# Kernel optimization log

Measured on AMD Instinct MI355X. Metric: run time of the kernel, lower is better.

The kernel has to match this reference:

```python
import jax, jax.numpy as jnp
import numpy as np
from jax import lax

SIGMA = 10.0


def _maxpool3(x):
    # x: (1, N, D, H, W), kernel 3, stride 1, VALID
    return lax.reduce_window(x, -jnp.inf, lax.max,
                             (1, 1, 3, 3, 3), (1, 1, 1, 1, 1), 'VALID')


def _avgpool3(x):
    s = lax.reduce_window(x, 0.0, lax.add,
                          (1, 1, 3, 3, 3), (1, 1, 1, 1, 1), 'VALID')
    return s / 27.0


def _smooth(x):
    # ReplicationPad3d(3) -> MaxPool3d(3,1) -> AvgPool3d(3,1) x2 ; keeps spatial size
    x = jnp.pad(x, ((0, 0), (0, 0), (3, 3), (3, 3), (3, 3)), mode='edge')
    return _avgpool3(_avgpool3(_maxpool3(x)))


def setup_inputs() -> dict:
    key = jax.random.key(0)
    k1, k2, k3 = jax.random.split(key, 3)
    N, K, L = 10000, 8, 13
    cost = jax.random.normal(k1, (N, 1, L, L, L), dtype=jnp.float32)
    knn = jax.random.randint(k2, (N, K), 0, N)
    dist_nn = jax.random.uniform(k3, (N, K), dtype=jnp.float32) * 20.0
    alpha = jnp.array([1.0, 0.1, 1.0, 1.0, 0.1, 1.0], dtype=jnp.float32)
    return {"cost": cost, "knn": knn, "dist_nn": dist_nn, "alpha": alpha}


def reference(cost, knn, dist_nn, alpha):
    N = cost.shape[0]
    L = cost.shape[2]
    cost = alpha[1] + alpha[0] * cost                       # (N,1,L,L,L)
    w = jnp.exp(-dist_nn / (2.0 * SIGMA ** 2))              # (N,K)
    norm = w.sum(axis=1)                                    # (N,)
    cost = cost.reshape(1, N, L, L, L)

    cost_approx = _smooth(cost)                             # (1,N,L,L,L)
    # gather K neighbors and do distance-weighted mean
    nbr = cost_approx[:, knn]                               # (1,N,K,L,L,L)
    cost_approx = jnp.einsum('ankxyz,nk->anxyz', nbr, w)
    cost_approx = cost_approx / norm[None, :, None, None, None]

    cost = alpha[4] + alpha[2] * cost + alpha[3] * cost_approx
    cost = _smooth(cost)
    nbr = cost[:, knn]                                      # (1,N,K,L,L,L)
    cost = jnp.einsum('ankxyz,nk->anxyz', nbr, w)
    cost = cost / norm[None, :, None, None, None]
    return alpha[5] * cost.reshape(1, N, -1)
```

## Files before the change

### kernel.cpp

```cpp
#include <hip/hip_runtime.h>
#include <math.h>

#define L3 2197
#define SP 2200
#define NV (SP / 8)
#define NTW 64
#define NTO 320

#define SSZ 3760

typedef unsigned int u32;

__device__ __forceinline__ u32 pack2bf(float a, float b) {
    u32 ua = __float_as_uint(a);
    u32 ub = __float_as_uint(b);
    ua = (ua + 0x7fffu + ((ua >> 16) & 1u)) >> 16;
    ub = (ub + 0x7fffu + ((ub >> 16) & 1u)) & 0xffff0000u;
    return ua | ub;
}

__device__ __forceinline__ void unpack8(uint4 v, float* f) {
    f[0] = __uint_as_float(v.x << 16);
    f[1] = __uint_as_float(v.x & 0xffff0000u);
    f[2] = __uint_as_float(v.y << 16);
    f[3] = __uint_as_float(v.y & 0xffff0000u);
    f[4] = __uint_as_float(v.z << 16);
    f[5] = __uint_as_float(v.z & 0xffff0000u);
    f[6] = __uint_as_float(v.w << 16);
    f[7] = __uint_as_float(v.w & 0xffff0000u);
}

__device__ __forceinline__ uint4 pack8(const float* f) {
    uint4 v;
    v.x = pack2bf(f[0], f[1]);
    v.y = pack2bf(f[2], f[3]);
    v.z = pack2bf(f[4], f[5]);
    v.w = pack2bf(f[6], f[7]);
    return v;
}

__device__ __forceinline__ void maxpool_row(const float* x, float* o) {
    float p[12];
#pragma unroll
    for (int i = 0; i < 12; ++i) p[i] = fmaxf(x[i], x[i + 1]);
    o[0] = x[0];
    o[1] = x[0];
    o[2] = p[0];
#pragma unroll
    for (int j = 3; j <= 13; ++j) o[j] = fmaxf(p[j - 3], x[j - 1]);
    o[14] = p[11];
    o[15] = x[12];
    o[16] = x[12];
}

__device__ __forceinline__ void tri_row(const float* y, float* o, float scale) {
#pragma unroll
    for (int c = 0; c < 13; ++c) {
        float s = fmaf(2.0f, y[c + 1], y[c]);
        s = fmaf(3.0f, y[c + 2], s);
        s = fmaf(2.0f, y[c + 3], s);
        o[c] = (s + y[c + 4]) * scale;
    }
}

__device__ void smooth_wave(float* S, const int lane) {
    __syncthreads();
#pragma unroll
    for (int cb = 2; cb >= 0; --cb) {
        const int p = cb * 64 + lane;
        const bool act = p < 169;
        float x[13], o[17];
        if (act) {
            const float* s = S + p * 13;
#pragma unroll
            for (int i = 0; i < 13; ++i) x[i] = s[i];
            maxpool_row(x, o);
        }
        __builtin_amdgcn_sched_barrier(0);
        if (act) {
            float* d = S + p * 17;
#pragma unroll
            for (int i = 0; i < 17; ++i) d[i] = o[i];
        }
        __builtin_amdgcn_sched_barrier(0);
    }
    __syncthreads();
#pragma unroll
    for (int cb = 3; cb >= 0; --cb) {
        const int p = cb * 64 + lane;
        const bool act = p < 221;
        const int a = p / 17, c = p % 17;
        float x[13], o[17];
        if (act) {
            const float* s = S + a * 221 + c;
#pragma unroll
            for (int i = 0; i < 13; ++i) x[i] = s[i * 17];
            maxpool_row(x, o);
        }
        __builtin_amdgcn_sched_barrier(0);
        if (act) {
            float* d = S + a * 289 + c;
#pragma unroll
            for (int i = 0; i < 17; ++i) d[i * 17] = o[i];
        }
        __builtin_amdgcn_sched_barrier(0);
    }
    __syncthreads();
#pragma unroll
    for (int cb = 0; cb < 5; ++cb) {
        const int p = cb * 64 + lane;
        if (p < 289) {
            float x[13], m[17], o[13];
            const float* s = S + p;
#pragma unroll
            for (int i = 0; i < 13; ++i) x[i] = s[i * 289];
            maxpool_row(x, m);
            tri_row(m, o, 1.0f);
            float* d = S + p;
#pragma unroll
            for (int i = 0; i < 13; ++i) d[i * 289] = o[i];
        }
    }
    __syncthreads();
#pragma unroll
    for (int cb = 0; cb < 4; ++cb) {
        const int p = cb * 64 + lane;
        const bool act = p < 221;
        const int a = p / 17, c = p % 17;
        float y[17], o[13];
        if (act) {
            const float* s = S + a * 289 + c;
#pragma unroll
            for (int i = 0; i < 17; ++i) y[i] = s[i * 17];
            tri_row(y, o, 1.0f);
        }
        __builtin_amdgcn_sched_barrier(0);
        if (act) {
            float* d = S + a * 221 + c;
#pragma unroll
            for (int i = 0; i < 13; ++i) d[i * 17] = o[i];
        }
        __builtin_amdgcn_sched_barrier(0);
    }
    __syncthreads();
#pragma unroll
    for (int cb = 0; cb < 3; ++cb) {
        const int p = cb * 64 + lane;
        const bool act = p < 169;
        float y[17], o[13];
        if (act) {
            const float* s = S + p * 17;
#pragma unroll
            for (int i = 0; i < 17; ++i) y[i] = s[i];
            tri_row(y, o, 1.0f / 729.0f);
        }
        __builtin_amdgcn_sched_barrier(0);
        if (act) {
            float* d = S + p * 13;
#pragma unroll
            for (int i = 0; i < 13; ++i) d[i] = o[i];
        }
        __builtin_amdgcn_sched_barrier(0);
    }
    __syncthreads();
}

__device__ __forceinline__ void load_nbr_meta(
        const int* __restrict__ knn, const float* __restrict__ dist,
        int n, int K, int* idx, float* wk, float* norm_out) {
    float dv[8];
#pragma unroll
    for (int k = 0; k < 8; ++k) {
        const int kc = (k < K) ? k : (K - 1);
        idx[k] = knn[n * K + kc];
        dv[k] = dist[n * K + kc];
    }
    float norm = 0.0f;
#pragma unroll
    for (int k = 0; k < 8; ++k) {
        float w = (k < K) ? expf(-dv[k] * (1.0f / 200.0f)) : 0.0f;
        wk[k] = w;
        norm += w;
    }
    *norm_out = norm;
}

__global__ __launch_bounds__(NTW) void k_smooth1(
        const float* __restrict__ cost, const float* __restrict__ alpha,
        uint4* __restrict__ tmp1, uint4* __restrict__ preA) {
    __shared__ alignas(16) float S[SSZ];
    const int n = blockIdx.x;
    const int lane = threadIdx.x;
    const float a0 = alpha[0], a1 = alpha[1], a2 = alpha[2], a4 = alpha[4];
    const float* src = cost + (size_t)n * L3;
    for (int i = lane; i < L3; i += NTW) S[i] = fmaf(a0, src[i], a1);
    if (lane < SP - L3) S[L3 + lane] = 0.0f;
    __syncthreads();
    uint4* pre = preA + (size_t)n * NV;
#pragma unroll
    for (int r = 0; r < 5; ++r) {
        const int i = r * 64 + lane;
        if (i < NV) {
            float f[8];
#pragma unroll
            for (int j = 0; j < 8; ++j) f[j] = fmaf(a2, S[8 * i + j], a4);
            pre[i] = pack8(f);
        }
    }
    smooth_wave(S, lane);
    uint4* dst = tmp1 + (size_t)n * NV;
#pragma unroll
    for (int r = 0; r < 5; ++r) {
        const int i = r * 64 + lane;
        if (i < NV) {
            float f[8];
            const int base = 8 * i;
#pragma unroll
            for (int j = 0; j < 8; ++j) f[j] = (base + j < L3) ? S[base + j] : 0.0f;
            dst[i] = pack8(f);
        }
    }
}

__global__ __launch_bounds__(NTW) void k_mid(
        const int* __restrict__ knn, const float* __restrict__ dist,
        const float* __restrict__ alpha, const uint4* __restrict__ tmp1,
        const uint4* __restrict__ preA, uint4* __restrict__ tmp2, int K) {
    __shared__ alignas(16) float S[SSZ];
    const int n = blockIdx.x;
    const int lane = threadIdx.x;
    int idx[8];
    float wk[8], norm;
    load_nbr_meta(knn, dist, n, K, idx, wk, &norm);
    const float sc = alpha[3] / norm;

    const uint4* pre = preA + (size_t)n * NV;
    const uint4* nb[8];
#pragma unroll
    for (int k = 0; k < 8; ++k)
        nb[k] = tmp1 + (size_t)__builtin_amdgcn_readfirstlane(idx[k]) * NV;

    uint4 av[9], bv[9];
    {
        const int i = lane;
        av[8] = pre[i];
#pragma unroll
        for (int k = 0; k < 8; ++k) av[k] = nb[k][i];
    }
#pragma unroll
    for (int r = 0; r < 5; ++r) {
        if (r < 4) {
            const int i = (r + 1) * 64 + lane;
            const int ic = (i < NV) ? i : (NV - 1);
            bv[8] = pre[ic];
#pragma unroll
            for (int k = 0; k < 8; ++k) bv[k] = nb[k][ic];
        }
        const int i = r * 64 + lane;
        if (i < NV) {
            float f[8], acc[8], g[8];
            unpack8(av[8], f);
#pragma unroll
            for (int j = 0; j < 8; ++j) acc[j] = 0.0f;
#pragma unroll
            for (int k = 0; k < 8; ++k) {
                unpack8(av[k], g);
#pragma unroll
                for (int j = 0; j < 8; ++j) acc[j] = fmaf(wk[k], g[j], acc[j]);
            }
#pragma unroll
            for (int j = 0; j < 8; ++j) S[8 * i + j] = fmaf(sc, acc[j], f[j]);
        }
#pragma unroll
        for (int q = 0; q < 9; ++q) av[q] = bv[q];
    }
    smooth_wave(S, lane);
    uint4* dst = tmp2 + (size_t)n * NV;
#pragma unroll
    for (int r = 0; r < 5; ++r) {
        const int i = r * 64 + lane;
        if (i < NV) {
            float f[8];
            const int base = 8 * i;
#pragma unroll
            for (int j = 0; j < 8; ++j) f[j] = (base + j < L3) ? S[base + j] : 0.0f;
            dst[i] = pack8(f);
        }
    }
}

__global__ __launch_bounds__(NTO) void k_out(
        const int* __restrict__ knn, const float* __restrict__ dist,
        const float* __restrict__ alpha, const uint4* __restrict__ tmp2,
        float* __restrict__ out, int K) {
    const int n = blockIdx.x;
    const int tid = threadIdx.x;
    int idx[8];
    float wk[8], norm;
    load_nbr_meta(knn, dist, n, K, idx, wk, &norm);
    const float sc = alpha[5] / norm;

    float* dst = out + (size_t)n * L3;
    if (tid < NV) {
        uint4 v[8];
#pragma unroll
        for (int k = 0; k < 8; ++k) {
            const size_t b = (size_t)__builtin_amdgcn_readfirstlane(idx[k]) * NV;
            v[k] = tmp2[b + tid];
        }
        float acc[8], g[8];
#pragma unroll
        for (int j = 0; j < 8; ++j) acc[j] = 0.0f;
#pragma unroll
        for (int k = 0; k < 8; ++k) {
            unpack8(v[k], g);
#pragma unroll
            for (int j = 0; j < 8; ++j) acc[j] = fmaf(wk[k], g[j], acc[j]);
        }
        const int base = 8 * tid;
#pragma unroll
        for (int j = 0; j < 8; ++j)
            if (base + j < L3) dst[base + j] = sc * acc[j];
    }
}

extern "C" void kernel_launch(void* const* d_in, const int* in_sizes, int n_in,
                              void* d_out, int out_size, void* d_ws, size_t ws_size,
                              hipStream_t stream) {
    const float* cost  = (const float*)d_in[0];
    const int*   knn   = (const int*)d_in[1];
    const float* dist  = (const float*)d_in[2];
    const float* alpha = (const float*)d_in[3];
    float* out = (float*)d_out;

    const int N = in_sizes[0] / L3;
    int K = in_sizes[1] / N;
    if (K > 8) K = 8;

    uint4* tmp1 = (uint4*)d_ws;
    uint4* tmp2 = tmp1 + (size_t)N * NV;
    uint4* preA = tmp2 + (size_t)N * NV;

    k_smooth1<<<N, NTW, 0, stream>>>(cost, alpha, tmp1, preA);
    k_mid<<<N, NTW, 0, stream>>>(knn, dist, alpha, tmp1, preA, tmp2, K);
    k_out<<<N, NTO, 0, stream>>>(knn, dist, alpha, tmp2, out, K);
}
```

Before: 339.4 us.

## Pad LDS rows to 18 floats and process column pairs with float2 accesses

Reworks the separable smoothing passes so intermediate rows use a stride of 18 floats. This lets each thread handle two adjacent columns using float2 LDS loads and stores, which halves the thread count for the middle passes. The first smooth kernel now reads cost directly from global memory inside the first pass instead of staging it in LDS, and the final packing uses float4 LDS reads. The trade-offs are more registers per thread, fewer active lanes in some passes, and a slightly larger LDS footprint.

```diff
diff --git a/kernel.cpp b/kernel.cpp
--- a/kernel.cpp
+++ b/kernel.cpp
@@ -7,7 +7,7 @@
 #define NTW 64
 #define NTO 320
 
-#define SSZ 3760
+#define SSZ 3984
 
 typedef unsigned int u32;
 
@@ -63,7 +63,8 @@
     }
 }
 
-__device__ void smooth_wave(float* S, const int lane) {
+__device__ void smooth_wave2(float* S, const int lane,
+                             const float* __restrict__ gsrc, float ga, float gb) {
     __syncthreads();
 #pragma unroll
     for (int cb = 2; cb >= 0; --cb) {
@@ -71,74 +72,96 @@
         const bool act = p < 169;
         float x[13], o[17];
         if (act) {
-            const float* s = S + p * 13;
-#pragma unroll
-            for (int i = 0; i < 13; ++i) x[i] = s[i];
+            if (gsrc != nullptr) {
+#pragma unroll
+                for (int i = 0; i < 13; ++i) x[i] = fmaf(ga, gsrc[p * 13 + i], gb);
+            } else {
+#pragma unroll
+                for (int i = 0; i < 13; ++i) x[i] = S[p * 13 + i];
+            }
             maxpool_row(x, o);
         }
         __builtin_amdgcn_sched_barrier(0);
         if (act) {
-            float* d = S + p * 17;
-#pragma unroll
-            for (int i = 0; i < 17; ++i) d[i] = o[i];
-        }
-        __builtin_amdgcn_sched_barrier(0);
-    }
-    __syncthreads();
-#pragma unroll
-    for (int cb = 3; cb >= 0; --cb) {
-        const int p = cb * 64 + lane;
-        const bool act = p < 221;
-        const int a = p / 17, c = p % 17;
-        float x[13], o[17];
-        if (act) {
-            const float* s = S + a * 221 + c;
-#pragma unroll
-            for (int i = 0; i < 13; ++i) x[i] = s[i * 17];
-            maxpool_row(x, o);
-        }
-        __builtin_amdgcn_sched_barrier(0);
-        if (act) {
-            float* d = S + a * 289 + c;
-#pragma unroll
-            for (int i = 0; i < 17; ++i) d[i * 17] = o[i];
-        }
-        __builtin_amdgcn_sched_barrier(0);
-    }
-    __syncthreads();
-#pragma unroll
-    for (int cb = 0; cb < 5; ++cb) {
-        const int p = cb * 64 + lane;
-        if (p < 289) {
-            float x[13], m[17], o[13];
-            const float* s = S + p;
-#pragma unroll
-            for (int i = 0; i < 13; ++i) x[i] = s[i * 289];
-            maxpool_row(x, m);
-            tri_row(m, o, 1.0f);
-            float* d = S + p;
-#pragma unroll
-            for (int i = 0; i < 13; ++i) d[i * 289] = o[i];
-        }
-    }
-    __syncthreads();
-#pragma unroll
-    for (int cb = 0; cb < 4; ++cb) {
-        const int p = cb * 64 + lane;
-        const bool act = p < 221;
-        const int a = p / 17, c = p % 17;
-        float y[17], o[13];
-        if (act) {
-            const float* s = S + a * 289 + c;
-#pragma unroll
-            for (int i = 0; i < 17; ++i) y[i] = s[i * 17];
-            tri_row(y, o, 1.0f);
-        }
-        __builtin_amdgcn_sched_barrier(0);
-        if (act) {
-            float* d = S + a * 221 + c;
-#pragma unroll
-            for (int i = 0; i < 13; ++i) d[i * 17] = o[i];
+            float* row = S + p * 18;
+#pragma unroll
+            for (int j = 0; j < 8; ++j)
+                *(float2*)(row + 2 * j) = make_float2(o[2 * j], o[2 * j + 1]);
+            row[16] = o[16];
+        }
+        __builtin_amdgcn_sched_barrier(0);
+    }
+    __syncthreads();
+#pragma unroll
+    for (int cb = 1; cb >= 0; --cb) {
+        const int q = cb * 64 + lane;
+        const bool act = q < 117;
+        const int a = q / 9, cp = q % 9;
+        float xl[13], xh[13], ol[17], oh[17];
+        if (act) {
+            const float* s = S + a * 234 + 2 * cp;
+#pragma unroll
+            for (int i = 0; i < 13; ++i) {
+                float2 v = *(const float2*)(s + i * 18);
+                xl[i] = v.x; xh[i] = v.y;
+            }
+            maxpool_row(xl, ol);
+            maxpool_row(xh, oh);
+        }
+        __builtin_amdgcn_sched_barrier(0);
+        if (act) {
+            float* d = S + a * 306 + 2 * cp;
+#pragma unroll
+            for (int i = 0; i < 17; ++i)
+                *(float2*)(d + i * 18) = make_float2(ol[i], oh[i]);
+        }
+        __builtin_amdgcn_sched_barrier(0);
+    }
+    __syncthreads();
+#pragma unroll
+    for (int cb = 0; cb < 3; ++cb) {
+        const int r = cb * 64 + lane;
+        if (r < 153) {
+            const int bp = r / 9, cp = r % 9;
+            float* colp = S + bp * 18 + 2 * cp;
+            float xl[13], xh[13], ml[17], mh[17], ol[13], oh[13];
+#pragma unroll
+            for (int i = 0; i < 13; ++i) {
+                float2 v = *(const float2*)(colp + i * 306);
+                xl[i] = v.x; xh[i] = v.y;
+            }
+            maxpool_row(xl, ml);
+            tri_row(ml, ol, 1.0f);
+            maxpool_row(xh, mh);
+            tri_row(mh, oh, 1.0f);
+#pragma unroll
+            for (int i = 0; i < 13; ++i)
+                *(float2*)(colp + i * 306) = make_float2(ol[i], oh[i]);
+        }
+    }
+    __syncthreads();
+#pragma unroll
+    for (int cb = 0; cb < 2; ++cb) {
+        const int q = cb * 64 + lane;
+        const bool act = q < 117;
+        const int a = q / 9, cp = q % 9;
+        float yl[17], yh[17], ol[13], oh[13];
+        if (act) {
+            const float* s = S + a * 306 + 2 * cp;
+#pragma unroll
+            for (int i = 0; i < 17; ++i) {
+                float2 v = *(const float2*)(s + i * 18);
+                yl[i] = v.x; yh[i] = v.y;
+            }
+            tri_row(yl, ol, 1.0f);
+            tri_row(yh, oh, 1.0f);
+        }
+        __builtin_amdgcn_sched_barrier(0);
+        if (act) {
+            float* d = S + a * 234 + 2 * cp;
+#pragma unroll
+            for (int i = 0; i < 13; ++i)
+                *(float2*)(d + i * 18) = make_float2(ol[i], oh[i]);
         }
         __builtin_amdgcn_sched_barrier(0);
     }
@@ -149,9 +172,13 @@
         const bool act = p < 169;
         float y[17], o[13];
         if (act) {
-            const float* s = S + p * 17;
-#pragma unroll
-            for (int i = 0; i < 17; ++i) y[i] = s[i];
+            const float* row = S + p * 18;
+#pragma unroll
+            for (int j = 0; j < 8; ++j) {
+                float2 v = *(const float2*)(row + 2 * j);
+                y[2 * j] = v.x; y[2 * j + 1] = v.y;
+            }
+            y[16] = row[16];
             tri_row(y, o, 1.0f / 729.0f);
         }
         __builtin_amdgcn_sched_barrier(0);
@@ -162,6 +189,7 @@
         }
         __builtin_amdgcn_sched_barrier(0);
     }
+    if (lane < SP - L3) S[L3 + lane] = 0.0f;
     __syncthreads();
 }
 
@@ -193,31 +221,34 @@
     const int lane = threadIdx.x;
     const float a0 = alpha[0], a1 = alpha[1], a2 = alpha[2], a4 = alpha[4];
     const float* src = cost + (size_t)n * L3;
-    for (int i = lane; i < L3; i += NTW) S[i] = fmaf(a0, src[i], a1);
-    if (lane < SP - L3) S[L3 + lane] = 0.0f;
-    __syncthreads();
+
     uint4* pre = preA + (size_t)n * NV;
 #pragma unroll
     for (int r = 0; r < 5; ++r) {
-        const int i = r * 64 + lane;
-        if (i < NV) {
+        const int t = r * 64 + lane;
+        if (t < NV) {
             float f[8];
 #pragma unroll
-            for (int j = 0; j < 8; ++j) f[j] = fmaf(a2, S[8 * i + j], a4);
-            pre[i] = pack8(f);
-        }
-    }
-    smooth_wave(S, lane);
+            for (int j = 0; j < 8; ++j) {
+                const int m = 8 * t + j;
+                const float c = (m < L3) ? src[m] : 0.0f;
+                f[j] = fmaf(a2, fmaf(a0, c, a1), a4);
+            }
+            pre[t] = pack8(f);
+        }
+    }
+
+    smooth_wave2(S, lane, src, a0, a1);
+
     uint4* dst = tmp1 + (size_t)n * NV;
+    const float4* Sv = (const float4*)S;
 #pragma unroll
     for (int r = 0; r < 5; ++r) {
-        const int i = r * 64 + lane;
-        if (i < NV) {
-            float f[8];
-            const int base = 8 * i;
-#pragma unroll
-            for (int j = 0; j < 8; ++j) f[j] = (base + j < L3) ? S[base + j] : 0.0f;
-            dst[i] = pack8(f);
+        const int t = r * 64 + lane;
+        if (t < NV) {
+            float4 f0 = Sv[2 * t], f1 = Sv[2 * t + 1];
+            float f[8] = {f0.x, f0.y, f0.z, f0.w, f1.x, f1.y, f1.z, f1.w};
+            dst[t] = pack8(f);
         }
     }
 }
@@ -240,6 +271,7 @@
     for (int k = 0; k < 8; ++k)
         nb[k] = tmp1 + (size_t)__builtin_amdgcn_readfirstlane(idx[k]) * NV;
 
+    float4* Sw = (float4*)S;
     uint4 av[9], bv[9];
     {
         const int i = lane;
@@ -268,23 +300,25 @@
 #pragma unroll
                 for (int j = 0; j < 8; ++j) acc[j] = fmaf(wk[k], g[j], acc[j]);
             }
-#pragma unroll
-            for (int j = 0; j < 8; ++j) S[8 * i + j] = fmaf(sc, acc[j], f[j]);
+            float rle[8];
+#pragma unroll
+            for (int j = 0; j < 8; ++j) rle[j] = fmaf(sc, acc[j], f[j]);
+            Sw[2 * i]     = make_float4(rle[0], rle[1], rle[2], rle[3]);
+            Sw[2 * i + 1] = make_float4(rle[4], rle[5], rle[6], rle[7]);
         }
 #pragma unroll
         for (int q = 0; q < 9; ++q) av[q] = bv[q];
     }
-    smooth_wave(S, lane);
+    smooth_wave2(S, lane, nullptr, 0.0f, 0.0f);
     uint4* dst = tmp2 + (size_t)n * NV;
+    const float4* Sv = (const float4*)S;
 #pragma unroll
     for (int r = 0; r < 5; ++r) {
-        const int i = r * 64 + lane;
-        if (i < NV) {
-            float f[8];
-            const int base = 8 * i;
-#pragma unroll
-            for (int j = 0; j < 8; ++j) f[j] = (base + j < L3) ? S[base + j] : 0.0f;
-            dst[i] = pack8(f);
+        const int t = r * 64 + lane;
+        if (t < NV) {
+            float4 f0 = Sv[2 * t], f1 = Sv[2 * t + 1];
+            float f[8] = {f0.x, f0.y, f0.z, f0.w, f1.x, f1.y, f1.z, f1.w};
+            dst[t] = pack8(f);
         }
     }
 }
```

Result: faster. 331.0 us (-2.5%).
